# Performance work log

Measured on AMD Instinct MI355X. Metric: run time of the kernel, lower is better.

Reference implementation:

```python
import jax, jax.numpy as jnp
import numpy as np

N_USER, N_ITEM, D = 100000, 50000, 64
H, S, B, L, SUPP, E, HID = 4, 500, 1024, 50, 10000, 1500000, 64

def setup_inputs() -> dict:
    key = jax.random.key(0)
    ks = jax.random.split(key, 24)
    f = lambda k, shp: (jax.random.normal(k, shp, jnp.float32) * 0.1)
    inp = {
        'x': jax.random.randint(ks[0], (B, 2), 0, 50000),
        'history': jax.random.randint(ks[1], (B, L), 0, N_ITEM),
        'history_len': jax.random.randint(ks[2], (B,), 1, L + 1),
        'sample_index': jax.random.randint(ks[3], (H, B, S), 0, SUPP),
        'supp_users': jax.random.randint(ks[4], (SUPP,), 0, N_USER),
        'edge_index': jax.random.randint(ks[5], (2, E), 0, 50000),
        'user_embedding': f(ks[6], (N_USER, D)),
        'item_embedding': f(ks[7], (N_ITEM, D)),
        'wq': f(ks[8], (H, D, D)),
        'wk': f(ks[9], (H, D, D)),
        'wv': f(ks[10], (H, D, D)),
        'w_out_w': f(ks[11], (H * D, D)),
        'gcn_user_w': f(ks[12], (D, D)), 'gcn_user_b': jnp.full((D,), 0.1, jnp.float32),
        'gcn_item_w': f(ks[13], (D, D)), 'gcn_item_b': jnp.full((D,), 0.1, jnp.float32),
        'l1_w': f(ks[14], (4 * D, 2 * HID)), 'l1_b': jnp.full((2 * HID,), 0.1, jnp.float32),
        'l2_w': f(ks[15], (2 * HID, HID)), 'l2_b': jnp.full((HID,), 0.1, jnp.float32),
        'l3_w': f(ks[16], (HID, 1)), 'l3_b': jnp.full((1,), 0.1, jnp.float32),
        'user_bias': jnp.zeros((N_USER, 1), jnp.float32),
        'item_bias': jnp.zeros((N_ITEM, 1), jnp.float32),
    }
    return inp


def _forward(x, history, history_len, sample_index, supp_users, edge_index,
             user_embedding, item_embedding, wq, wk, wv, w_out_w,
             gcn_user_w, gcn_user_b, gcn_item_w, gcn_item_b,
             l1_w, l1_b, l2_w, l2_b, l3_w, l3_b, user_bias, item_bias):
    user_id = x[:, 0]
    item_id = x[:, 1]
    # user init embedding: mean of history item embeddings (original sums unmasked, divides by len)
    user_init_emb = jnp.sum(item_embedding[history], axis=1) / history_len[:, None].astype(jnp.float32)  # [B,D]

    # multi-head RelationGAT over randomly sampled support users
    samp_emb = user_embedding[supp_users[sample_index]]            # [H,B,S,D]
    q = jnp.einsum('bd,hde->hbe', user_init_emb, wq)               # [H,B,D]
    k = jnp.einsum('hbsd,hde->hbse', samp_emb, wk)                 # [H,B,S,D]
    attn = jax.nn.softmax(jnp.einsum('hbe,hbse->hbs', q, k), axis=-1)
    ctx = jnp.einsum('hbs,hbse->hbe', attn, k)                     # [H,B,D]
    gat = jnp.einsum('hbe,hef->hbf', ctx, wv)                      # [H,B,D]
    gat = jnp.transpose(gat, (1, 0, 2)).reshape(gat.shape[1], -1)  # [B,H*D]
    user_emb = gat @ w_out_w                                       # [B,D]

    item_emb = item_embedding[item_id]

    # sparse GCN aggregation via segment_sum (eval mode: no edge dropout)
    eu, ei = edge_index[0], edge_index[1]
    ones_e = jnp.ones((eu.shape[0],), jnp.float32)
    agg_item = jax.ops.segment_sum(item_embedding[ei], eu, num_segments=N_USER)[user_id]
    agg_user = jax.ops.segment_sum(user_embedding[eu], ei, num_segments=N_ITEM)[item_id]
    deg_u = jax.ops.segment_sum(ones_e, eu, num_segments=N_USER)[user_id][:, None] + 1.0
    deg_i = jax.ops.segment_sum(ones_e, ei, num_segments=N_ITEM)[item_id][:, None] + 1.0
    gcn_item_h = agg_item / deg_u
    gcn_user_h = agg_user / deg_i
    gcn_user_out = jax.nn.relu(gcn_user_h @ gcn_user_w + gcn_user_b)
    gcn_item_out = jax.nn.relu(gcn_item_h @ gcn_item_w + gcn_item_b)

    feats = jnp.concatenate([user_emb * item_emb,
                             user_emb * gcn_item_out,
                             gcn_user_out * item_emb,
                             gcn_user_out * gcn_item_out], axis=-1)  # [B,4D]
    h1 = jnp.tanh(feats @ l1_w + l1_b)
    h2 = jnp.tanh(h1 @ l2_w + l2_b)
    score = (h2 @ l3_w + l3_b).reshape(-1)
    return score + user_bias[user_id].reshape(-1) + item_bias[item_id].reshape(-1)


def reference(x, history, history_len, sample_index, supp_users, edge_index,
              user_embedding, item_embedding, wq, wk, wv, w_out_w,
              gcn_user_w, gcn_user_b, gcn_item_w, gcn_item_b,
              l1_w, l1_b, l2_w, l2_b, l3_w, l3_b, user_bias, item_bias):
    return _forward(x, history, history_len, sample_index, supp_users, edge_index,
                    user_embedding, item_embedding, wq, wk, wv, w_out_w,
                    gcn_user_w, gcn_user_b, gcn_item_w, gcn_item_b,
                    l1_w, l1_b, l2_w, l2_b, l3_w, l3_b, user_bias, item_bias)
```

## Files before the change

kernel.cpp:

```cpp
#include <hip/hip_runtime.h>
#include <hip/hip_bf16.h>
#include <math.h>

#define N_USER 100000
#define N_ITEM 50000
#define D 64
#define H 4
#define S 500
#define B 1024
#define L 50
#define SUPP 10000
#define E_EDGES 1500000
#define HID 64
#define N_ID 50000
#define CAP 256

#define SUPP_BLKS 625
#define UINIT_BLKS 256
#define PREP1_BLKS 32
#define PREP2_BLKS 64
#define REP_BLKS 4
#define B_UINIT (SUPP_BLKS)
#define B_PREP1 (B_UINIT + UINIT_BLKS)
#define B_PREP2 (B_PREP1 + PREP1_BLKS)
#define B_REP   (B_PREP2 + PREP2_BLKS)
#define SETUP_BLKS (B_REP + REP_BLKS)

__device__ __forceinline__ ushort f2bf(float f) {
  unsigned u = __float_as_uint(f);
  return (ushort)((u + 0x7FFF + ((u >> 16) & 1)) >> 16);
}
__device__ __forceinline__ float bf_lo(unsigned v) { return __uint_as_float(v << 16); }
__device__ __forceinline__ float bf_hi(unsigned v) { return __uint_as_float(v & 0xFFFF0000u); }

__global__ void k_setup(const int* x, const int* history, const int* history_len,
                        const int* supp_users, const float* user_embedding,
                        const float* item_embedding, const float* wq, const float* wk,
                        const float* wv, const float* w_out_w,
                        ushort* supp_bf, float* uinit, float* Mmat, float* Pmat,
                        int* user_rep, int* item_rep, int* uctr, int* ictr) {
  __shared__ float smem[64 * 65];
  int blk = blockIdx.x, tid = threadIdx.x;
  if (blk < B_UINIT) {
    int i = blk * 256 + tid;
    if (i < SUPP * 16) {
      int r = i >> 4, c = i & 15;
      float4 v = *(const float4*)&user_embedding[(long)supp_users[r] * 64 + c * 4];
      ushort4 o = {f2bf(v.x), f2bf(v.y), f2bf(v.z), f2bf(v.w)};
      *(ushort4*)&supp_bf[r * 64 + c * 4] = o;
    }
  } else if (blk < B_PREP1) {
    int b = (blk - B_UINIT) * 4 + (tid >> 6);
    int lane = tid & 63, g = lane >> 4, sub = lane & 15;
    float4 acc = {0.f, 0.f, 0.f, 0.f};
    for (int l = g; l < L; l += 4) {
      int idx = history[b * L + l];
      float4 r = *(const float4*)&item_embedding[(long)idx * 64 + sub * 4];
      acc.x += r.x; acc.y += r.y; acc.z += r.z; acc.w += r.w;
    }
    acc.x += __shfl_xor(acc.x, 16); acc.y += __shfl_xor(acc.y, 16);
    acc.z += __shfl_xor(acc.z, 16); acc.w += __shfl_xor(acc.w, 16);
    acc.x += __shfl_xor(acc.x, 32); acc.y += __shfl_xor(acc.y, 32);
    acc.z += __shfl_xor(acc.z, 32); acc.w += __shfl_xor(acc.w, 32);
    if (lane < 16) {
      float inv = 1.f / (float)history_len[b];
      float4 o = {acc.x * inv, acc.y * inv, acc.z * inv, acc.w * inv};
      *(float4*)&uinit[b * 64 + lane * 4] = o;
    }
  } else if (blk < B_PREP2) {
    int local = blk - B_PREP1;
    int h = local >> 3, bx = local & 7;
    for (int i = tid; i < 64 * 64; i += 256) {
      int row = i >> 6, e = i & 63;
      smem[row * 65 + e] = wk[((long)h * 64 + row) * 64 + e];
    }
    __syncthreads();
    for (int k = 0; k < 2; k++) {
      int oidx = bx * 512 + k * 256 + tid;
      int dp = oidx >> 6, d = oidx & 63;
      float acc = 0.f;
      const float* wqrow = wq + ((long)h * 64 + dp) * 64;
#pragma unroll
      for (int e = 0; e < 64; e++) acc += wqrow[e] * smem[d * 65 + e];
      Mmat[((long)h * 64 + dp) * 64 + d] = acc;
    }
  } else if (blk < B_REP) {
    int local = blk - B_PREP2;
    int p = tid >> 6, lane = tid & 63;
    int gp = local * 4 + p;
    int h = gp >> 6, row = gp & 63;
    float* T = smem + p * 64;
    float tf = 0.f;
#pragma unroll
    for (int e = 0; e < 64; e++)
      tf += wk[((long)h * 64 + row) * 64 + e] * wv[((long)h * 64 + e) * 64 + lane];
    T[lane] = tf;
    __syncthreads();
    float acc = 0.f;
#pragma unroll
    for (int f = 0; f < 64; f++)
      acc += T[f] * w_out_w[((long)h * 64 + f) * 64 + lane];
    Pmat[((long)h * 64 + row) * 64 + lane] = acc;
  } else {
    int gi = (blk - B_REP) * 256 + tid;
    if (gi < B) {
      user_rep[x[2 * gi]] = gi;
      item_rep[x[2 * gi + 1]] = gi;
      uctr[gi] = 0;
      ictr[gi] = 0;
    }
  }
}

template <int CTRL>
__device__ __forceinline__ float dpp_add(float v) {
  int t = __builtin_amdgcn_update_dpp(0, __float_as_int(v), CTRL, 0xF, 0xF, true);
  return v + __int_as_float(t);
}
#define DPP_XOR1  0xB1
#define DPP_XOR2  0x4E
#define DPP_ROR4  0x124
#define DPP_ROR8  0x128

#define MID_EDGE ((E_EDGES / 4 + 255) / 256)
#define MID_BLKS (MID_EDGE + B * H)

__device__ __forceinline__ void edge_probe(int u, int it, const int* x,
                                           const int* user_rep, const int* item_rep,
                                           int* uctr, int* ubin, int* ictr, int* ibin) {
  int ru = user_rep[u];
  if ((unsigned)ru < B && x[2 * ru] == u) {
    int pos = atomicAdd(&uctr[ru], 1);
    if (pos < CAP) ubin[ru * CAP + pos] = it;
  }
  int ri = item_rep[it];
  if ((unsigned)ri < B && x[2 * ri + 1] == it) {
    int pos = atomicAdd(&ictr[ri], 1);
    if (pos < CAP) ibin[ri * CAP + pos] = u;
  }
}

__global__ void k_mid(const int* eu, const int* ei, const int* x,
                      const int* user_rep, const int* item_rep,
                      int* uctr, int* ubin, int* ictr, int* ibin,
                      const float* uinit, const ushort* supp_bf, const int* sample_index,
                      const float* Mmat, const float* Pmat, float* uem4) {
  int tid = threadIdx.x;
  if (blockIdx.x < MID_EDGE) {
    int i = blockIdx.x * 256 + tid;
    if (i >= E_EDGES / 4) return;
    int4 u4 = ((const int4*)eu)[i];
    int4 v4 = ((const int4*)ei)[i];
    edge_probe(u4.x, v4.x, x, user_rep, item_rep, uctr, ubin, ictr, ibin);
    edge_probe(u4.y, v4.y, x, user_rep, item_rep, uctr, ubin, ictr, ibin);
    edge_probe(u4.z, v4.z, x, user_rep, item_rep, uctr, ubin, ictr, ibin);
    edge_probe(u4.w, v4.w, x, user_rep, item_rep, uctr, ubin, ictr, ibin);
    return;
  }
  int id = blockIdx.x - MID_EDGE;
  int h = id >> 10, b = id & 1023;
  int w = tid >> 6, lane = tid & 63;
  int g = lane >> 4, sub = lane & 15;
  __shared__ float sm_u[64], sm_kq[64], sm_p[256], sm_part[256], sm_den[4];
  __shared__ int sm_sidx[512];

  const int* sidx = sample_index + ((long)h * B + b) * S;
  for (int i = tid; i < 512; i += 256) sm_sidx[i] = (i < S) ? sidx[i] : 0;
  if (tid < 64) sm_u[tid] = uinit[b * 64 + tid];
  __syncthreads();

  const float* Mh = Mmat + h * 64 * 64;
  {
    float p = 0.f;
#pragma unroll
    for (int j = 0; j < 16; j++) p += sm_u[w * 16 + j] * Mh[(w * 16 + j) * 64 + lane];
    sm_p[tid] = p;
  }
  __syncthreads();
  if (tid < 64) sm_kq[tid] = sm_p[tid] + sm_p[64 + tid] + sm_p[128 + tid] + sm_p[192 + tid];
  __syncthreads();

  float4 kq4 = *(float4*)&sm_kq[sub * 4];
  float4 acc = {0.f, 0.f, 0.f, 0.f};
  float den = 0.f;
#pragma unroll 4
  for (int it = 0; it < 32; it++) {
    int s = it * 16 + w * 4 + g;
    int idx = sm_sidx[s];
    uint2 rv = *(const uint2*)&supp_bf[idx * 64 + sub * 4];
    float r0 = bf_lo(rv.x), r1 = bf_hi(rv.x), r2 = bf_lo(rv.y), r3 = bf_hi(rv.y);
    float dot = r0 * kq4.x + r1 * kq4.y + r2 * kq4.z + r3 * kq4.w;
    dot = dpp_add<DPP_XOR1>(dot);
    dot = dpp_add<DPP_XOR2>(dot);
    dot = dpp_add<DPP_ROR4>(dot);
    dot = dpp_add<DPP_ROR8>(dot);
    float e = (s < S) ? __expf(dot) : 0.f;
    den += e;
    acc.x += e * r0; acc.y += e * r1; acc.z += e * r2; acc.w += e * r3;
  }
  den += __shfl_xor(den, 16); den += __shfl_xor(den, 32);
  acc.x += __shfl_xor(acc.x, 16); acc.y += __shfl_xor(acc.y, 16);
  acc.z += __shfl_xor(acc.z, 16); acc.w += __shfl_xor(acc.w, 16);
  acc.x += __shfl_xor(acc.x, 32); acc.y += __shfl_xor(acc.y, 32);
  acc.z += __shfl_xor(acc.z, 32); acc.w += __shfl_xor(acc.w, 32);
  if (lane < 16) {
    *(float4*)&sm_part[w * 64 + lane * 4] = acc;
    if (lane == 0) sm_den[w] = den;
  }
  __syncthreads();
  if (tid < 64) {
    float ws_ = sm_part[tid] + sm_part[64 + tid] + sm_part[128 + tid] + sm_part[192 + tid];
    float dn = sm_den[0] + sm_den[1] + sm_den[2] + sm_den[3];
    sm_u[tid] = ws_ / dn;
  }
  __syncthreads();
  const float* Ph = Pmat + h * 64 * 64;
  {
    float p = 0.f;
#pragma unroll
    for (int j = 0; j < 16; j++) p += sm_u[w * 16 + j] * Ph[(w * 16 + j) * 64 + lane];
    sm_p[tid] = p;
  }
  __syncthreads();
  if (tid < 64)
    uem4[((long)h * B + b) * 64 + tid] =
        sm_p[tid] + sm_p[64 + tid] + sm_p[128 + tid] + sm_p[192 + tid];
}

__global__ void k_final(const int* x, const float* uem4,
                        const float* user_embedding, const float* item_embedding,
                        const int* user_rep, const int* item_rep,
                        const int* uctr, const int* ubin, const int* ictr, const int* ibin,
                        const float* gcn_user_w, const float* gcn_user_b,
                        const float* gcn_item_w, const float* gcn_item_b,
                        const float* l1_w, const float* l1_b,
                        const float* l2_w, const float* l2_b,
                        const float* l3_w, const float* l3_b,
                        const float* user_bias, const float* item_bias, float* out) {
  int b = blockIdx.x, tid = threadIdx.x;
  int side = tid >> 6, lane = tid & 63;
  __shared__ float ue[D], ie[D], agg[2][D], degs[2], guo[D], gio[D],
      feats[4 * D], h1[2 * HID], h2[HID];
  int uid = x[2 * b], iid = x[2 * b + 1];

  {
    int rep = side == 0 ? user_rep[uid] : item_rep[iid];
    int cnt = min((side == 0 ? uctr : ictr)[rep], CAP);
    const int* bin = ((side == 0 ? ubin : ibin)) + rep * CAP;
    const float* emb = side == 0 ? item_embedding : user_embedding;
    float s0 = 0.f, s1 = 0.f, s2 = 0.f, s3 = 0.f;
    int m = 0;
    for (; m + 3 < cnt; m += 4) {
      s0 += emb[(long)bin[m] * 64 + lane];
      s1 += emb[(long)bin[m + 1] * 64 + lane];
      s2 += emb[(long)bin[m + 2] * 64 + lane];
      s3 += emb[(long)bin[m + 3] * 64 + lane];
    }
    for (; m < cnt; m++) s0 += emb[(long)bin[m] * 64 + lane];
    agg[side][lane] = (s0 + s1) + (s2 + s3);
    if (lane == 0) degs[side] = (float)cnt;
  }
  if (tid < D) {
    ue[tid] = uem4[(0L * B + b) * D + tid] + uem4[(1L * B + b) * D + tid] +
              uem4[(2L * B + b) * D + tid] + uem4[(3L * B + b) * D + tid];
    ie[tid] = item_embedding[(long)iid * D + tid];
  }
  __syncthreads();
  if (tid < D) {
    float gih = agg[0][tid] / (degs[0] + 1.f);
    float guh = agg[1][tid] / (degs[1] + 1.f);
    agg[0][tid] = gih;
    agg[1][tid] = guh;
  }
  __syncthreads();
  if (tid < D) {
    float a = 0.f, c = 0.f;
    for (int d = 0; d < D; d++) {
      a += agg[1][d] * gcn_user_w[d * D + tid];
      c += agg[0][d] * gcn_item_w[d * D + tid];
    }
    guo[tid] = fmaxf(a + gcn_user_b[tid], 0.f);
    gio[tid] = fmaxf(c + gcn_item_b[tid], 0.f);
  }
  __syncthreads();
  if (tid < D) {
    feats[tid]         = ue[tid] * ie[tid];
    feats[D + tid]     = ue[tid] * gio[tid];
    feats[2 * D + tid] = guo[tid] * ie[tid];
    feats[3 * D + tid] = guo[tid] * gio[tid];
  }
  __syncthreads();
  {
    float a = 0.f;
    for (int i = 0; i < 4 * D; i++) a += feats[i] * l1_w[i * (2 * HID) + tid];
    h1[tid] = tanhf(a + l1_b[tid]);
  }
  __syncthreads();
  if (tid < HID) {
    float a = 0.f;
    for (int i = 0; i < 2 * HID; i++) a += h1[i] * l2_w[i * HID + tid];
    h2[tid] = tanhf(a + l2_b[tid]);
  }
  __syncthreads();
  if (tid < 64) {
    float v = h2[tid] * l3_w[tid];
#pragma unroll
    for (int off = 32; off > 0; off >>= 1) v += __shfl_xor(v, off);
    if (tid == 0)
      out[b] = v + l3_b[0] + user_bias[uid] + item_bias[iid];
  }
}

extern "C" void kernel_launch(void* const* d_in, const int* in_sizes, int n_in,
                              void* d_out, int out_size, void* d_ws, size_t ws_size,
                              hipStream_t stream) {
  const int* x             = (const int*)d_in[0];
  const int* history       = (const int*)d_in[1];
  const int* history_len   = (const int*)d_in[2];
  const int* sample_index  = (const int*)d_in[3];
  const int* supp_users    = (const int*)d_in[4];
  const int* edge_index    = (const int*)d_in[5];
  const float* user_embedding = (const float*)d_in[6];
  const float* item_embedding = (const float*)d_in[7];
  const float* wq       = (const float*)d_in[8];
  const float* wk       = (const float*)d_in[9];
  const float* wv       = (const float*)d_in[10];
  const float* w_out_w  = (const float*)d_in[11];
  const float* gcn_user_w = (const float*)d_in[12];
  const float* gcn_user_b = (const float*)d_in[13];
  const float* gcn_item_w = (const float*)d_in[14];
  const float* gcn_item_b = (const float*)d_in[15];
  const float* l1_w = (const float*)d_in[16];
  const float* l1_b = (const float*)d_in[17];
  const float* l2_w = (const float*)d_in[18];
  const float* l2_b = (const float*)d_in[19];
  const float* l3_w = (const float*)d_in[20];
  const float* l3_b = (const float*)d_in[21];
  const float* user_bias = (const float*)d_in[22];
  const float* item_bias = (const float*)d_in[23];
  float* out = (float*)d_out;

  float* fws        = (float*)d_ws;
  float* uinit      = fws;
  ushort* supp_bf   = (ushort*)(uinit + B * D);
  float* uem4       = uinit + B * D + SUPP * D / 2;
  float* Mmat       = uem4 + (long)H * B * D;
  float* Pmat       = Mmat + H * D * D;
  int* user_rep     = (int*)(Pmat + H * D * D);
  int* item_rep     = user_rep + N_ID;
  int* uctr         = item_rep + N_ID;
  int* ictr         = uctr + B;
  int* ubin         = ictr + B;
  int* ibin         = ubin + B * CAP;

  const int* eu = edge_index;
  const int* ei = edge_index + E_EDGES;

  k_setup<<<SETUP_BLKS, 256, 0, stream>>>(x, history, history_len, supp_users,
                                          user_embedding, item_embedding, wq, wk, wv,
                                          w_out_w, supp_bf, uinit, Mmat, Pmat,
                                          user_rep, item_rep, uctr, ictr);
  k_mid<<<MID_BLKS, 256, 0, stream>>>(eu, ei, x, user_rep, item_rep,
                                      uctr, ubin, ictr, ibin,
                                      uinit, supp_bf, sample_index, Mmat, Pmat, uem4);
  k_final<<<B, 128, 0, stream>>>(x, uem4, user_embedding, item_embedding,
                                 user_rep, item_rep, uctr, ubin, ictr, ibin,
                                 gcn_user_w, gcn_user_b, gcn_item_w, gcn_item_b,
                                 l1_w, l1_b, l2_w, l2_b, l3_w, l3_b,
                                 user_bias, item_bias, out);
}
```

Before: 76.94 us.

## Store support embeddings as fp16 and use packed dot2 in attention

The staged support-user embedding table is now stored in fp16 instead of bf16. The attention inner loop has each lane load 8 halves (16 bytes), computes the score with fdot2 instructions, and reduces across 8 lanes with three DPP steps instead of four. The block order in k_mid is also swapped so attention blocks are scheduled before the edge-probe blocks. This targets the instruction count of the gather-and-dot loop. In exchange fp16 has less exponent range than bf16, which the small-magnitude embeddings should tolerate, and each lane now holds more accumulator registers.

```diff
diff --git a/kernel.cpp b/kernel.cpp
--- a/kernel.cpp
+++ b/kernel.cpp
@@ -15,6 +15,8 @@
 #define N_ID 50000
 #define CAP 256
 
+typedef _Float16 half2v __attribute__((ext_vector_type(2)));
+
 #define SUPP_BLKS 625
 #define UINIT_BLKS 256
 #define PREP1_BLKS 32
@@ -26,18 +28,16 @@
 #define B_REP   (B_PREP2 + PREP2_BLKS)
 #define SETUP_BLKS (B_REP + REP_BLKS)
 
-__device__ __forceinline__ ushort f2bf(float f) {
-  unsigned u = __float_as_uint(f);
-  return (ushort)((u + 0x7FFF + ((u >> 16) & 1)) >> 16);
-}
-__device__ __forceinline__ float bf_lo(unsigned v) { return __uint_as_float(v << 16); }
-__device__ __forceinline__ float bf_hi(unsigned v) { return __uint_as_float(v & 0xFFFF0000u); }
+__device__ __forceinline__ ushort f2h(float f) {
+  _Float16 h = (_Float16)f;
+  return __builtin_bit_cast(ushort, h);
+}
 
 __global__ void k_setup(const int* x, const int* history, const int* history_len,
                         const int* supp_users, const float* user_embedding,
                         const float* item_embedding, const float* wq, const float* wk,
                         const float* wv, const float* w_out_w,
-                        ushort* supp_bf, float* uinit, float* Mmat, float* Pmat,
+                        ushort* supp_h, float* uinit, float* Mmat, float* Pmat,
                         int* user_rep, int* item_rep, int* uctr, int* ictr) {
   __shared__ float smem[64 * 65];
   int blk = blockIdx.x, tid = threadIdx.x;
@@ -46,8 +46,8 @@
     if (i < SUPP * 16) {
       int r = i >> 4, c = i & 15;
       float4 v = *(const float4*)&user_embedding[(long)supp_users[r] * 64 + c * 4];
-      ushort4 o = {f2bf(v.x), f2bf(v.y), f2bf(v.z), f2bf(v.w)};
-      *(ushort4*)&supp_bf[r * 64 + c * 4] = o;
+      ushort4 o = {f2h(v.x), f2h(v.y), f2h(v.z), f2h(v.w)};
+      *(ushort4*)&supp_h[r * 64 + c * 4] = o;
     }
   } else if (blk < B_PREP1) {
     int b = (blk - B_UINIT) * 4 + (tid >> 6);
@@ -119,11 +119,28 @@
 }
 #define DPP_XOR1  0xB1
 #define DPP_XOR2  0x4E
-#define DPP_ROR4  0x124
-#define DPP_ROR8  0x128
-
+#define DPP_HMIR  0x141
+
+__device__ __forceinline__ float dot8h(uint4 rv, half2v k0, half2v k1, half2v k2, half2v k3) {
+#if __has_builtin(__builtin_amdgcn_fdot2)
+  float d = __builtin_amdgcn_fdot2(__builtin_bit_cast(half2v, rv.x), k0, 0.f, false);
+  d = __builtin_amdgcn_fdot2(__builtin_bit_cast(half2v, rv.y), k1, d, false);
+  d = __builtin_amdgcn_fdot2(__builtin_bit_cast(half2v, rv.z), k2, d, false);
+  d = __builtin_amdgcn_fdot2(__builtin_bit_cast(half2v, rv.w), k3, d, false);
+  return d;
+#else
+  half2v a = __builtin_bit_cast(half2v, rv.x), b = __builtin_bit_cast(half2v, rv.y);
+  half2v c = __builtin_bit_cast(half2v, rv.z), e = __builtin_bit_cast(half2v, rv.w);
+  return (float)a[0] * (float)k0[0] + (float)a[1] * (float)k0[1] +
+         (float)b[0] * (float)k1[0] + (float)b[1] * (float)k1[1] +
+         (float)c[0] * (float)k2[0] + (float)c[1] * (float)k2[1] +
+         (float)e[0] * (float)k3[0] + (float)e[1] * (float)k3[1];
+#endif
+}
+
+#define MID_ATTN (B * H)
 #define MID_EDGE ((E_EDGES / 4 + 255) / 256)
-#define MID_BLKS (MID_EDGE + B * H)
+#define MID_BLKS (MID_ATTN + MID_EDGE)
 
 __device__ __forceinline__ void edge_probe(int u, int it, const int* x,
                                            const int* user_rep, const int* item_rep,
@@ -143,11 +160,11 @@
 __global__ void k_mid(const int* eu, const int* ei, const int* x,
                       const int* user_rep, const int* item_rep,
                       int* uctr, int* ubin, int* ictr, int* ibin,
-                      const float* uinit, const ushort* supp_bf, const int* sample_index,
+                      const float* uinit, const ushort* supp_h, const int* sample_index,
                       const float* Mmat, const float* Pmat, float* uem4) {
   int tid = threadIdx.x;
-  if (blockIdx.x < MID_EDGE) {
-    int i = blockIdx.x * 256 + tid;
+  if (blockIdx.x >= MID_ATTN) {
+    int i = (blockIdx.x - MID_ATTN) * 256 + tid;
     if (i >= E_EDGES / 4) return;
     int4 u4 = ((const int4*)eu)[i];
     int4 v4 = ((const int4*)ei)[i];
@@ -157,10 +174,10 @@
     edge_probe(u4.w, v4.w, x, user_rep, item_rep, uctr, ubin, ictr, ibin);
     return;
   }
-  int id = blockIdx.x - MID_EDGE;
+  int id = blockIdx.x;
   int h = id >> 10, b = id & 1023;
   int w = tid >> 6, lane = tid & 63;
-  int g = lane >> 4, sub = lane & 15;
+  int g8 = lane >> 3, sub8 = lane & 7;
   __shared__ float sm_u[64], sm_kq[64], sm_p[256], sm_part[256], sm_den[4];
   __shared__ int sm_sidx[512];
 
@@ -180,31 +197,47 @@
   if (tid < 64) sm_kq[tid] = sm_p[tid] + sm_p[64 + tid] + sm_p[128 + tid] + sm_p[192 + tid];
   __syncthreads();
 
-  float4 kq4 = *(float4*)&sm_kq[sub * 4];
-  float4 acc = {0.f, 0.f, 0.f, 0.f};
+  float4 kqa = *(float4*)&sm_kq[sub8 * 8];
+  float4 kqb = *(float4*)&sm_kq[sub8 * 8 + 4];
+  half2v k0 = {(_Float16)kqa.x, (_Float16)kqa.y};
+  half2v k1 = {(_Float16)kqa.z, (_Float16)kqa.w};
+  half2v k2 = {(_Float16)kqb.x, (_Float16)kqb.y};
+  half2v k3 = {(_Float16)kqb.z, (_Float16)kqb.w};
+
+  float acc[8] = {0.f, 0.f, 0.f, 0.f, 0.f, 0.f, 0.f, 0.f};
   float den = 0.f;
 #pragma unroll 4
-  for (int it = 0; it < 32; it++) {
-    int s = it * 16 + w * 4 + g;
+  for (int it = 0; it < 16; it++) {
+    int s = it * 32 + w * 8 + g8;
     int idx = sm_sidx[s];
-    uint2 rv = *(const uint2*)&supp_bf[idx * 64 + sub * 4];
-    float r0 = bf_lo(rv.x), r1 = bf_hi(rv.x), r2 = bf_lo(rv.y), r3 = bf_hi(rv.y);
-    float dot = r0 * kq4.x + r1 * kq4.y + r2 * kq4.z + r3 * kq4.w;
+    uint4 rv = *(const uint4*)&supp_h[idx * 64 + sub8 * 8];
+    float dot = dot8h(rv, k0, k1, k2, k3);
     dot = dpp_add<DPP_XOR1>(dot);
     dot = dpp_add<DPP_XOR2>(dot);
-    dot = dpp_add<DPP_ROR4>(dot);
-    dot = dpp_add<DPP_ROR8>(dot);
+    dot = dpp_add<DPP_HMIR>(dot);
     float e = (s < S) ? __expf(dot) : 0.f;
     den += e;
-    acc.x += e * r0; acc.y += e * r1; acc.z += e * r2; acc.w += e * r3;
-  }
-  den += __shfl_xor(den, 16); den += __shfl_xor(den, 32);
-  acc.x += __shfl_xor(acc.x, 16); acc.y += __shfl_xor(acc.y, 16);
-  acc.z += __shfl_xor(acc.z, 16); acc.w += __shfl_xor(acc.w, 16);
-  acc.x += __shfl_xor(acc.x, 32); acc.y += __shfl_xor(acc.y, 32);
-  acc.z += __shfl_xor(acc.z, 32); acc.w += __shfl_xor(acc.w, 32);
-  if (lane < 16) {
-    *(float4*)&sm_part[w * 64 + lane * 4] = acc;
+    half2v r0 = __builtin_bit_cast(half2v, rv.x);
+    half2v r1 = __builtin_bit_cast(half2v, rv.y);
+    half2v r2 = __builtin_bit_cast(half2v, rv.z);
+    half2v r3 = __builtin_bit_cast(half2v, rv.w);
+    acc[0] += e * (float)r0[0]; acc[1] += e * (float)r0[1];
+    acc[2] += e * (float)r1[0]; acc[3] += e * (float)r1[1];
+    acc[4] += e * (float)r2[0]; acc[5] += e * (float)r2[1];
+    acc[6] += e * (float)r3[0]; acc[7] += e * (float)r3[1];
+  }
+#pragma unroll
+  for (int j = 0; j < 8; j++) {
+    acc[j] += __shfl_xor(acc[j], 8);
+    acc[j] += __shfl_xor(acc[j], 16);
+    acc[j] += __shfl_xor(acc[j], 32);
+  }
+  den += __shfl_xor(den, 8); den += __shfl_xor(den, 16); den += __shfl_xor(den, 32);
+  if (lane < 8) {
+    float4 lo = {acc[0], acc[1], acc[2], acc[3]};
+    float4 hi = {acc[4], acc[5], acc[6], acc[7]};
+    *(float4*)&sm_part[w * 64 + lane * 8] = lo;
+    *(float4*)&sm_part[w * 64 + lane * 8 + 4] = hi;
     if (lane == 0) sm_den[w] = den;
   }
   __syncthreads();
@@ -342,7 +375,7 @@
 
   float* fws        = (float*)d_ws;
   float* uinit      = fws;
-  ushort* supp_bf   = (ushort*)(uinit + B * D);
+  ushort* supp_h    = (ushort*)(uinit + B * D);
   float* uem4       = uinit + B * D + SUPP * D / 2;
   float* Mmat       = uem4 + (long)H * B * D;
   float* Pmat       = Mmat + H * D * D;
@@ -358,11 +391,11 @@
 
   k_setup<<<SETUP_BLKS, 256, 0, stream>>>(x, history, history_len, supp_users,
                                           user_embedding, item_embedding, wq, wk, wv,
-                                          w_out_w, supp_bf, uinit, Mmat, Pmat,
+                                          w_out_w, supp_h, uinit, Mmat, Pmat,
                                           user_rep, item_rep, uctr, ictr);
   k_mid<<<MID_BLKS, 256, 0, stream>>>(eu, ei, x, user_rep, item_rep,
                                       uctr, ubin, ictr, ibin,
-                                      uinit, supp_bf, sample_index, Mmat, Pmat, uem4);
+                                      uinit, supp_h, sample_index, Mmat, Pmat, uem4);
   k_final<<<B, 128, 0, stream>>>(x, uem4, user_embedding, item_embedding,
                                  user_rep, item_rep, uctr, ubin, ictr, ibin,
                                  gcn_user_w, gcn_user_b, gcn_item_w, gcn_item_b,
```

Result: no change. 75.70 us (-1.6%).
